# Performance work log

Measured on AMD Instinct MI355X. Metric: run time of the kernel, lower is better.

Reference implementation:

```python
import jax, jax.numpy as jnp
import numpy as np

K = 32           # neighbors per point
HEADS = 8
EPS = 1e-5       # BatchNorm eps
NEG_SLOPE = 0.2  # LeakyReLU slope


def knn_idx(x, k):
    # x: (B, C, N) -> (B, N, k) indices of k nearest neighbors in feature space
    xx = jnp.sum(x * x, axis=1)                       # (B, N)
    inner = jnp.einsum('bcn,bcm->bnm', x, x)          # (B, N, N)
    neg_sq_dist = 2.0 * inner - xx[:, :, None] - xx[:, None, :]
    return jax.lax.top_k(neg_sq_dist, k)[1]           # (B, N, k)


def group_diff(x, k):
    # DGCNN-style 'diff' grouping: neighbor features minus center feature.
    idx = knn_idx(x, k)                               # (B, N, k)
    xt = jnp.transpose(x, (0, 2, 1))                  # (B, N, C)
    nb = jax.vmap(lambda f, i: f[i])(xt, idx)         # (B, N, k, C)
    diff = nb - xt[:, :, None, :]                     # (B, N, k, C)
    return jnp.transpose(diff, (0, 3, 1, 2))          # (B, C, N, k)


def batchnorm1d(y, gamma, beta):
    # training-mode BN over (B, C, N): stats over batch and point dims
    m = jnp.mean(y, axis=(0, 2), keepdims=True)
    v = jnp.var(y, axis=(0, 2), keepdims=True)
    return gamma[None, :, None] * (y - m) * jax.lax.rsqrt(v + EPS) + beta[None, :, None]


def setup_inputs() -> dict:
    key = jax.random.key(0)
    ks = jax.random.split(key, 6)
    B, C, N = 8, 64, 2048
    return {
        'x':  jax.random.normal(ks[0], (B, C, N), jnp.float32),
        'Wq': jax.random.normal(ks[1], (64, 64), jnp.float32) * 0.1,
        'Wk': jax.random.normal(ks[2], (64, 64), jnp.float32) * 0.1,
        'Wv': jax.random.normal(ks[3], (64, 64), jnp.float32) * 0.1,
        'W1': jax.random.normal(ks[4], (128, 64), jnp.float32) * 0.1,
        'W2': jax.random.normal(ks[5], (64, 128), jnp.float32) * 0.1,
        'g1': jnp.ones((64,), jnp.float32),
        'b1': jnp.zeros((64,), jnp.float32),
        'g2': jnp.ones((64,), jnp.float32),
        'b2': jnp.zeros((64,), jnp.float32),
    }


def reference(x, Wq, Wk, Wv, W1, W2, g1, b1, g2, b2):
    B, C, N = x.shape
    nbr = group_diff(x, K)                                        # (B, C, N, K)

    # 1x1 conv projections == per-point matmuls
    q = jnp.einsum('oc,bcn->bon', Wq, x)                          # (B, Co, N)
    q = q.reshape(B, HEADS, -1, N).transpose(0, 1, 3, 2)          # (B, H, N, d)
    k = jnp.einsum('oc,bcnk->bonk', Wk, nbr)
    k = k.reshape(B, HEADS, -1, N, K).transpose(0, 1, 3, 4, 2)    # (B, H, N, K, d)
    v = jnp.einsum('oc,bcnk->bonk', Wv, nbr)
    v = v.reshape(B, HEADS, -1, N, K).transpose(0, 1, 3, 4, 2)    # (B, H, N, K, d)

    scale = jnp.sqrt(jnp.asarray(q.shape[-1], q.dtype))
    energy = jnp.einsum('bhnd,bhnkd->bhnk', q, k) / scale         # (B, H, N, K)
    attn = jax.nn.softmax(energy, axis=-1)
    out = jnp.einsum('bhnk,bhnkd->bhnd', attn, v)                 # (B, H, N, d)
    out = out.transpose(0, 2, 1, 3).reshape(B, N, -1).transpose(0, 2, 1)  # (B, Cv, N)

    x1 = batchnorm1d(x + out, g1, b1)
    h = jax.nn.leaky_relu(jnp.einsum('oc,bcn->bon', W1, x1), NEG_SLOPE)
    ff = jnp.einsum('oc,bcn->bon', W2, h)
    return batchnorm1d(x1 + ff, g2, b2)
```

## Files before the change

kernel.cpp:

```cpp
#include <hip/hip_runtime.h>


#define NN 2048

typedef __attribute__((ext_vector_type(8))) short bf16x8;
typedef __attribute__((ext_vector_type(8))) unsigned short u16x8;
typedef __attribute__((ext_vector_type(4))) float f32x4;

__device__ inline void bsplit(float x, short& h, short& m, short& l)
{
    unsigned u  = __float_as_uint(x);
    unsigned hb = (u + 0x7FFFu + ((u >> 16) & 1u)) >> 16;
    float hf = __uint_as_float(hb << 16);
    float r1 = x - hf;
    unsigned u1 = __float_as_uint(r1);
    unsigned mb = (u1 + 0x7FFFu + ((u1 >> 16) & 1u)) >> 16;
    float mf = __uint_as_float(mb << 16);
    float r2 = r1 - mf;
    unsigned u2 = __float_as_uint(r2);
    unsigned lb = (u2 + 0x7FFFu + ((u2 >> 16) & 1u)) >> 16;
    h = (short)hb; m = (short)mb; l = (short)lb;
}

__global__ __launch_bounds__(256) void prep_kernel(
    const float* __restrict__ x, const float* __restrict__ Wk,
    const float* __restrict__ Wv, float* __restrict__ xx,
    float* __restrict__ KT, float* __restrict__ VT,
    short* __restrict__ xh, short* __restrict__ xm, short* __restrict__ xl)
{
    __shared__ float xs[64][33];
    __shared__ float wks[4096], wvs[4096];
    const int t = threadIdx.x;
    const int b = blockIdx.x >> 6;
    const int n0 = (blockIdx.x & 63) * 32;
    for (int i = 0; i < 16; ++i) {
        int e = t + 256 * i;
        wks[e] = Wk[e];
        wvs[e] = Wv[e];
    }
    for (int i = 0; i < 8; ++i) {
        int e = t + 256 * i;
        xs[e >> 5][e & 31] = x[((size_t)b * 64 + (e >> 5)) * 2048 + n0 + (e & 31)];
    }
    __syncthreads();
    if (t < 32) {
        float s = 0.f;
#pragma unroll
        for (int c = 0; c < 64; ++c) { float v = xs[c][t]; s += v * v; }
        xx[b * 2048 + n0 + t] = s;
    }
    const int p = t & 31, g = t >> 5;
    {
        u16x8 vh, vm, vl;
#pragma unroll
        for (int ci = 0; ci < 8; ++ci) {
            short h, m, l;
            bsplit(xs[g * 8 + ci][p], h, m, l);
            vh[ci] = (unsigned short)h; vm[ci] = (unsigned short)m; vl[ci] = (unsigned short)l;
        }
        size_t base = ((size_t)(b * 2048 + n0 + p)) * 64 + g * 8;
        *reinterpret_cast<u16x8*>(xh + base) = vh;
        *reinterpret_cast<u16x8*>(xm + base) = vm;
        *reinterpret_cast<u16x8*>(xl + base) = vl;
    }
    {
        float xv[64];
#pragma unroll
        for (int c = 0; c < 64; ++c) xv[c] = xs[c][p];
        size_t base = ((size_t)(b * 2048 + n0 + p)) * 64 + g * 8;
        float ok[8], ov[8];
#pragma unroll
        for (int oi = 0; oi < 8; ++oi) {
            int o = g * 8 + oi;
            float ak = 0.f, av = 0.f;
#pragma unroll
            for (int c = 0; c < 64; ++c) {
                float xc = xv[c];
                ak += wks[o * 64 + c] * xc;
                av += wvs[o * 64 + c] * xc;
            }
            ok[oi] = ak; ov[oi] = av;
        }
        *reinterpret_cast<float4*>(KT + base)     = make_float4(ok[0], ok[1], ok[2], ok[3]);
        *reinterpret_cast<float4*>(KT + base + 4) = make_float4(ok[4], ok[5], ok[6], ok[7]);
        *reinterpret_cast<float4*>(VT + base)     = make_float4(ov[0], ov[1], ov[2], ov[3]);
        *reinterpret_cast<float4*>(VT + base + 4) = make_float4(ov[4], ov[5], ov[6], ov[7]);
    }
}

__device__ inline void mm6(f32x4& a, bf16x8 Ah, bf16x8 Am, bf16x8 Al,
                           bf16x8 Bh, bf16x8 Bm, bf16x8 Bl)
{
    a = __builtin_amdgcn_mfma_f32_16x16x32_bf16(Al, Bh, a, 0, 0, 0);
    a = __builtin_amdgcn_mfma_f32_16x16x32_bf16(Ah, Bl, a, 0, 0, 0);
    a = __builtin_amdgcn_mfma_f32_16x16x32_bf16(Am, Bm, a, 0, 0, 0);
    a = __builtin_amdgcn_mfma_f32_16x16x32_bf16(Am, Bh, a, 0, 0, 0);
    a = __builtin_amdgcn_mfma_f32_16x16x32_bf16(Ah, Bm, a, 0, 0, 0);
    a = __builtin_amdgcn_mfma_f32_16x16x32_bf16(Ah, Bh, a, 0, 0, 0);
}

__global__ __launch_bounds__(256) void gemm_kernel(
    const short* __restrict__ xh, const short* __restrict__ xm,
    const short* __restrict__ xl, const float* __restrict__ xx,
    float* __restrict__ Dp)
{
    __shared__ short BhL[8192], BmL[8192], BlL[8192];
    const int t = threadIdx.x;
    const int lane = t & 63;
    const int w = t >> 6;
    const int b = blockIdx.x >> 8;
    const int tile = blockIdx.x & 255;
    const int r0 = (tile >> 4) * 128 + w * 32;
    const int c0 = (tile & 15) * 128;
    const int rl = lane & 15;
    const int g = lane >> 4;
    const int kg = g * 8;

    const size_t boff = (size_t)b * 2048 * 64;
    const short* XH = xh + boff;
    const short* XM = xm + boff;
    const short* XL = xl + boff;

    bf16x8 aH[2][2], aM[2][2], aL[2][2];
#pragma unroll
    for (int s = 0; s < 2; ++s)
#pragma unroll
        for (int rb = 0; rb < 2; ++rb) {
            const size_t ab = (size_t)(r0 + rb * 16 + rl) * 64 + s * 32 + kg;
            aH[s][rb] = *reinterpret_cast<const bf16x8*>(XH + ab);
            aM[s][rb] = *reinterpret_cast<const bf16x8*>(XM + ab);
            aL[s][rb] = *reinterpret_cast<const bf16x8*>(XL + ab);
        }

    {
        const short* sH = XH + (size_t)c0 * 64;
        const short* sM = XM + (size_t)c0 * 64;
        const short* sL = XL + (size_t)c0 * 64;
#pragma unroll
        for (int i = 0; i < 4; ++i) {
            int ci = t + 256 * i;
            int col = ci >> 3, j = ci & 7;
            int d = col * 64 + ((j ^ (col & 7)) << 3);
            *reinterpret_cast<u16x8*>(BhL + d) = *reinterpret_cast<const u16x8*>(sH + ci * 8);
            *reinterpret_cast<u16x8*>(BmL + d) = *reinterpret_cast<const u16x8*>(sM + ci * 8);
            *reinterpret_cast<u16x8*>(BlL + d) = *reinterpret_cast<const u16x8*>(sL + ci * 8);
        }
    }
    __syncthreads();

    f32x4 acc[2][8];
#pragma unroll
    for (int rb = 0; rb < 2; ++rb)
#pragma unroll
        for (int cb = 0; cb < 8; ++cb)
            acc[rb][cb] = (f32x4){0.f, 0.f, 0.f, 0.f};

#pragma unroll
    for (int cb = 0; cb < 8; ++cb) {
        __builtin_amdgcn_sched_barrier(0);
        const int cl = cb * 16 + rl;
#pragma unroll
        for (int s = 0; s < 2; ++s) {
            const int d = cl * 64 + (((s * 4 + g) ^ (cl & 7)) << 3);
            bf16x8 Bh = *reinterpret_cast<const bf16x8*>(BhL + d);
            bf16x8 Bm = *reinterpret_cast<const bf16x8*>(BmL + d);
            bf16x8 Bl = *reinterpret_cast<const bf16x8*>(BlL + d);
            mm6(acc[0][cb], aH[s][0], aM[s][0], aL[s][0], Bh, Bm, Bl);
            mm6(acc[1][cb], aH[s][1], aM[s][1], aL[s][1], Bh, Bm, Bl);
        }
    }
    __builtin_amdgcn_sched_barrier(0);

    const float* xxb = xx + b * 2048;
    const int rg = g * 4;
#pragma unroll
    for (int cb = 0; cb < 8; ++cb) {
        const int col = c0 + cb * 16 + rl;
        const float xc = xxb[col];
#pragma unroll
        for (int rb = 0; rb < 2; ++rb) {
            const int rbase = r0 + rb * 16 + rg;
#pragma unroll
            for (int e = 0; e < 4; ++e) {
                float v = 2.f * acc[rb][cb][e] - xxb[rbase + e];
                v = v - xc;
                Dp[((size_t)(b * 2048 + rbase + e)) * 2048 + col] = v;
            }
        }
    }
}

__device__ inline unsigned long long sort64desc(unsigned long long v, int lane)
{
#pragma unroll
    for (int k = 2; k <= 64; k <<= 1) {
#pragma unroll
        for (int j = k >> 1; j > 0; j >>= 1) {
            unsigned long long o = (unsigned long long)__shfl_xor((long long)v, j);
            bool takeMax = (((lane & k) == 0) == ((lane & j) == 0));
            unsigned long long mx = v > o ? v : o;
            unsigned long long mn = v > o ? o : v;
            v = takeMax ? mx : mn;
        }
    }
    return v;
}

__global__ __launch_bounds__(512) void select_kernel(
    const float* __restrict__ Dp, int* __restrict__ idx)
{
    __shared__ unsigned long long cand[8][64];
    const int t = threadIdx.x, w = t >> 6, lane = t & 63;
    const int b = blockIdx.x >> 8;
    const int r = (blockIdx.x & 255) * 8 + w;
    const float* row = Dp + ((size_t)(b * 2048 + r)) * 2048;
    int* orow = idx + ((size_t)(b * 2048 + r)) * 32;

    const unsigned lobase = 2047u - (unsigned)(lane * 4);

    unsigned sv[32];
    unsigned qsv[8]; int qsl[8];
#pragma unroll
    for (int q = 0; q < 8; ++q) {
        float4 f = *reinterpret_cast<const float4*>(row + q * 256 + lane * 4);
        float vv[4] = {f.x, f.y, f.z, f.w};
#pragma unroll
        for (int e = 0; e < 4; ++e) {
            unsigned u = __float_as_uint(vv[e]);
            sv[q * 4 + e] = u ^ (unsigned)(((int)u >> 31) | 0x80000000);
        }
        unsigned v01 = sv[q * 4 + 1] > sv[q * 4] ? sv[q * 4 + 1] : sv[q * 4];
        int      s01 = sv[q * 4 + 1] > sv[q * 4] ? 1 : 0;
        unsigned v23 = sv[q * 4 + 3] > sv[q * 4 + 2] ? sv[q * 4 + 3] : sv[q * 4 + 2];
        int      s23 = sv[q * 4 + 3] > sv[q * 4 + 2] ? 3 : 2;
        qsv[q] = v23 > v01 ? v23 : v01;
        qsl[q] = q * 4 + (v23 > v01 ? s23 : s01);
    }
#pragma unroll
    for (int n = 4; n >= 1; n >>= 1)
#pragma unroll
        for (int i = 0; i < n; ++i) {
            bool take = qsv[i + n] > qsv[i];
            qsv[i] = take ? qsv[i + n] : qsv[i];
            qsl[i] = take ? qsl[i + n] : qsl[i];
        }
    const unsigned bsv = qsv[0];
    const int bs = qsl[0];
    const unsigned blo = lobase - (unsigned)(((bs >> 2) << 8) + (bs & 3));

    unsigned long long hk = ((unsigned long long)bsv << 32) | blo;
    unsigned long long hs = sort64desc(hk, lane);
    const unsigned long long Tkey = (unsigned long long)__shfl((long long)hs, 31);
    const unsigned Tsv = (unsigned)(Tkey >> 32);
    const unsigned Tlo = (unsigned)(Tkey & 0xFFFFFFFFu);

    int c = 0;
#pragma unroll
    for (int s = 0; s < 32; ++s) {
        unsigned lo = lobase - (unsigned)(((s >> 2) << 8) + (s & 3));
        bool ge = (sv[s] > Tsv) || (sv[s] == Tsv && lo >= Tlo);
        c += ge ? 1 : 0;
    }
    int pfx = c;
#pragma unroll
    for (int d = 1; d < 64; d <<= 1) {
        int o = __shfl_up(pfx, d);
        pfx += (lane >= d) ? o : 0;
    }
    const int total = __shfl(pfx, 63);
    int off = pfx - c;

    if (total <= 64) {
        if (lane >= total) cand[w][lane] = 0ull;
#pragma unroll
        for (int s = 0; s < 32; ++s) {
            unsigned lo = lobase - (unsigned)(((s >> 2) << 8) + (s & 3));
            bool ge = (sv[s] > Tsv) || (sv[s] == Tsv && lo >= Tlo);
            if (ge) cand[w][off++] = ((unsigned long long)sv[s] << 32) | lo;
        }
        asm volatile("s_waitcnt lgkmcnt(0)" ::: "memory");
        __builtin_amdgcn_sched_barrier(0);
        unsigned long long q = cand[w][lane];
        q = sort64desc(q, lane);
        if (lane < 32) orow[lane] = 2047 - (int)(q & 0xFFFFu);
    } else {
        unsigned cons = 0u;
        for (int it = 0; it < 32; ++it) {
            unsigned b2 = 0u, l2 = 0u;
#pragma unroll
            for (int s = 0; s < 32; ++s) {
                unsigned lo = lobase - (unsigned)(((s >> 2) << 8) + (s & 3));
                bool ok = !((cons >> s) & 1u) &&
                          ((sv[s] > b2) || (sv[s] == b2 && lo > l2));
                b2 = ok ? sv[s] : b2;
                l2 = ok ? lo : l2;
            }
            unsigned wsv = b2, wlo = l2;
#pragma unroll
            for (int d = 1; d < 64; d <<= 1) {
                unsigned osv = __shfl_xor(wsv, d);
                unsigned olo = __shfl_xor(wlo, d);
                bool take = (osv > wsv) || (osv == wsv && olo > wlo);
                wsv = take ? osv : wsv;
                wlo = take ? olo : wlo;
            }
            int gidx = 2047 - (int)wlo;
            if (lane == ((gidx >> 2) & 63)) {
                int slot = ((gidx >> 8) << 2) | (gidx & 3);
                cons |= 1u << slot;
            }
            if (lane == 0) orow[it] = gidx;
        }
    }
}

__global__ __launch_bounds__(256) void knn_kernel(
    const float* __restrict__ x, const float* __restrict__ xx,
    int* __restrict__ idx)
{
    __shared__ float Bs[64][65];
    __shared__ float As[4][65];
    __shared__ float xxs[2048];
    const int t = threadIdx.x, w = t >> 6, lane = t & 63;
    const int b = blockIdx.x >> 9;
    const int r0 = (blockIdx.x & 511) * 4;
    { int row = t >> 6, c = t & 63;
      As[row][c] = x[((size_t)b * 64 + c) * 2048 + r0 + row]; }
    for (int i = 0; i < 8; ++i) { int e = t + 256 * i; xxs[e] = xx[b * 2048 + e]; }
    const float xxr = xx[b * 2048 + r0 + w];
    float v[32];
    for (int jt = 0; jt < 32; ++jt) {
        __syncthreads();
        for (int i = 0; i < 16; ++i) {
            int e = t + 256 * i, c = e >> 6, p = e & 63;
            Bs[p][c] = x[((size_t)b * 64 + c) * 2048 + jt * 64 + p];
        }
        __syncthreads();
        float acc = 0.f;
#pragma unroll
        for (int c = 0; c < 64; ++c) acc += As[w][c] * Bs[lane][c];
        v[jt] = 2.f * acc - xxr - xxs[jt * 64 + lane];
    }
    unsigned mask = 0u;
    int* orow = idx + ((size_t)(b * 2048 + r0 + w)) * 32;
    for (int it = 0; it < 32; ++it) {
        float bv = -INFINITY; int bj = 0;
#pragma unroll
        for (int j = 0; j < 32; ++j) {
            bool ok = !((mask >> j) & 1u) && (v[j] > bv);
            bv = ok ? v[j] : bv;
            bj = ok ? j : bj;
        }
        int bi = bj * 64 + lane;
#pragma unroll
        for (int d = 1; d < 64; d <<= 1) {
            float ov = __shfl_xor(bv, d);
            int oi = __shfl_xor(bi, d);
            bool take = (ov > bv) || (ov == bv && oi < bi);
            bv = take ? ov : bv;
            bi = take ? oi : bi;
        }
        if (lane == (bi & 63)) mask |= 1u << (bi >> 6);
        if (lane == 0) orow[it] = bi;
    }
}

__global__ __launch_bounds__(256) void attn_kernel(
    const float* __restrict__ x, const float* __restrict__ Wq,
    const float* __restrict__ KT, const float* __restrict__ VT,
    const int* __restrict__ idx, float* __restrict__ A1)
{
    __shared__ float wq[64][65];
    __shared__ int idxs[32];
    __shared__ float xq[64];
    __shared__ float qs[64];
    __shared__ float Kn[32][66], Vn[32][66];
    __shared__ float es[256], av[256];
    const int t = threadIdx.x;
    const int b = blockIdx.x >> 11;
    const int n = blockIdx.x & 2047;
    const size_t pbase = ((size_t)(b * 2048 + n)) * 64;
    if (t < 32) idxs[t] = idx[((size_t)(b * 2048 + n)) * 32 + t] & 2047;
    else if (t < 96) xq[t - 32] = x[((size_t)b * 64 + (t - 32)) * 2048 + n];
    for (int i = 0; i < 16; ++i) {
        int e = t + 256 * i;
        wq[e >> 6][e & 63] = Wq[e];
    }
    __syncthreads();
    {
        int j = t >> 3, c0 = (t & 7) * 8;
        size_t nb = ((size_t)(b * 2048 + idxs[j])) * 64 + c0;
        float4 ka = *reinterpret_cast<const float4*>(KT + nb);
        float4 kb = *reinterpret_cast<const float4*>(KT + nb + 4);
        float4 va = *reinterpret_cast<const float4*>(VT + nb);
        float4 vb = *reinterpret_cast<const float4*>(VT + nb + 4);
        Kn[j][c0 + 0] = ka.x; Kn[j][c0 + 1] = ka.y; Kn[j][c0 + 2] = ka.z; Kn[j][c0 + 3] = ka.w;
        Kn[j][c0 + 4] = kb.x; Kn[j][c0 + 5] = kb.y; Kn[j][c0 + 6] = kb.z; Kn[j][c0 + 7] = kb.w;
        Vn[j][c0 + 0] = va.x; Vn[j][c0 + 1] = va.y; Vn[j][c0 + 2] = va.z; Vn[j][c0 + 3] = va.w;
        Vn[j][c0 + 4] = vb.x; Vn[j][c0 + 5] = vb.y; Vn[j][c0 + 6] = vb.z; Vn[j][c0 + 7] = vb.w;
    }
    if (t < 64) {
        float a = 0.f;
#pragma unroll
        for (int c = 0; c < 64; ++c) a += wq[t][c] * xq[c];
        qs[t] = a * 0.35355339059327379f;
    }
    __syncthreads();
    {
        int h = t >> 5, j = t & 31;
        float e = 0.f;
#pragma unroll
        for (int d = 0; d < 8; ++d) e += qs[h * 8 + d] * Kn[j][h * 8 + d];
        es[h * 32 + j] = e;
    }
    __syncthreads();
    if (t < 8) {
        float mx = -INFINITY;
#pragma unroll
        for (int j = 0; j < 32; ++j) mx = fmaxf(mx, es[t * 32 + j]);
        float pv[32], s = 0.f;
#pragma unroll
        for (int j = 0; j < 32; ++j) { pv[j] = __expf(es[t * 32 + j] - mx); s += pv[j]; }
        float inv = 1.f / s;
#pragma unroll
        for (int j = 0; j < 32; ++j) av[t * 32 + j] = pv[j] * inv;
    }
    __syncthreads();
    if (t < 64) {
        int h = t >> 3;
        float acc = 0.f;
#pragma unroll
        for (int j = 0; j < 32; ++j) acc += av[h * 32 + j] * Vn[j][t];
        A1[pbase + t] = acc - VT[pbase + t] + xq[t];
    }
}

__global__ __launch_bounds__(256) void bn_partial_kernel(
    const float* __restrict__ Y, float* __restrict__ psum, float* __restrict__ psq)
{
    __shared__ float rs[4][64], rq[4][64];
    const int t = threadIdx.x;
    const int c = t & 63, pg = t >> 6;
    const int b = blockIdx.x >> 3;
    const int n0 = (blockIdx.x & 7) * 256;
    float s = 0.f, q = 0.f;
    for (int k = 0; k < 64; ++k) {
        float v = Y[((size_t)(b * 2048 + n0 + pg * 64 + k)) * 64 + c];
        s += v; q += v * v;
    }
    rs[pg][c] = s; rq[pg][c] = q;
    __syncthreads();
    if (t < 64) {
        psum[blockIdx.x * 64 + t] = rs[0][t] + rs[1][t] + rs[2][t] + rs[3][t];
        psq[blockIdx.x * 64 + t]  = rq[0][t] + rq[1][t] + rq[2][t] + rq[3][t];
    }
}

__global__ void bn_final_kernel(
    const float* __restrict__ psum, const float* __restrict__ psq,
    const float* __restrict__ gamma, const float* __restrict__ beta,
    float* __restrict__ sc, float* __restrict__ sh)
{
    int c = threadIdx.x;
    float s = 0.f, q = 0.f;
    for (int i = 0; i < 64; ++i) { s += psum[i * 64 + c]; q += psq[i * 64 + c]; }
    float mean = s * (1.f / 16384.f);
    float var = q * (1.f / 16384.f) - mean * mean;
    float g = gamma[c] * rsqrtf(var + 1e-5f);
    sc[c] = g;
    sh[c] = beta[c] - mean * g;
}

__global__ __launch_bounds__(256) void ffn_kernel(
    const float* __restrict__ A1, const float* __restrict__ W1,
    const float* __restrict__ W2, const float* __restrict__ s1,
    const float* __restrict__ t1, float* __restrict__ P2)
{
    __shared__ float W1s[8192];
    __shared__ float W2s[8192];
    __shared__ float xs[64][65];
    __shared__ float hs[64][129];
    __shared__ float sts[64], stt[64];
    const int t = threadIdx.x;
    const int b = blockIdx.x >> 5;
    const int n0 = (blockIdx.x & 31) * 64;
    if (t < 64) { sts[t] = s1[t]; stt[t] = t1[t]; }
    for (int i = 0; i < 32; ++i) {
        int e = t + 256 * i;
        W1s[e] = W1[e];
        W2s[e] = W2[e];
    }
    __syncthreads();
    for (int i = 0; i < 16; ++i) {
        int e = t + 256 * i, p = e >> 6, c = e & 63;
        xs[p][c] = A1[((size_t)(b * 2048 + n0 + p)) * 64 + c] * sts[c] + stt[c];
    }
    __syncthreads();
    const int p = t & 63, g = t >> 6;
    {
        float xv[64];
#pragma unroll
        for (int c = 0; c < 64; ++c) xv[c] = xs[p][c];
        for (int u = 0; u < 32; ++u) {
            int j = g * 32 + u;
            float acc = 0.f;
#pragma unroll
            for (int c = 0; c < 64; ++c) acc += W1s[j * 64 + c] * xv[c];
            hs[p][j] = (acc > 0.f) ? acc : 0.2f * acc;
        }
    }
    __syncthreads();
    {
        float hv[128];
#pragma unroll
        for (int j = 0; j < 128; ++j) hv[j] = hs[p][j];
        const size_t pbase = ((size_t)(b * 2048 + n0 + p)) * 64 + g * 16;
        float o4[16];
#pragma unroll
        for (int oi = 0; oi < 16; ++oi) {
            int o = g * 16 + oi;
            float a = xs[p][o];
#pragma unroll
            for (int j = 0; j < 128; ++j) a += W2s[o * 128 + j] * hv[j];
            o4[oi] = a;
        }
#pragma unroll
        for (int q = 0; q < 4; ++q)
            *reinterpret_cast<float4*>(P2 + pbase + q * 4) =
                make_float4(o4[q * 4], o4[q * 4 + 1], o4[q * 4 + 2], o4[q * 4 + 3]);
    }
}

__global__ __launch_bounds__(256) void final_kernel(
    const float* __restrict__ P2, const float* __restrict__ s2,
    const float* __restrict__ t2, float* __restrict__ out)
{
    __shared__ float ts[64][65];
    __shared__ float sts[64], stt[64];
    const int t = threadIdx.x;
    const int b = blockIdx.x >> 5;
    const int n0 = (blockIdx.x & 31) * 64;
    if (t < 64) { sts[t] = s2[t]; stt[t] = t2[t]; }
    __syncthreads();
    for (int i = 0; i < 16; ++i) {
        int e = t + 256 * i, p = e >> 6, c = e & 63;
        ts[p][c] = P2[((size_t)(b * 2048 + n0 + p)) * 64 + c] * sts[c] + stt[c];
    }
    __syncthreads();
    const int c = t >> 2, p0 = (t & 3) * 16;
    float* dst = out + ((size_t)(b * 64 + c)) * 2048 + n0 + p0;
#pragma unroll
    for (int q = 0; q < 4; ++q)
        *reinterpret_cast<float4*>(dst + q * 4) =
            make_float4(ts[p0 + q * 4 + 0][c], ts[p0 + q * 4 + 1][c],
                        ts[p0 + q * 4 + 2][c], ts[p0 + q * 4 + 3][c]);
}

__global__ __launch_bounds__(256) void zero_kernel(float* __restrict__ out)
{
    reinterpret_cast<float4*>(out)[blockIdx.x * 256 + threadIdx.x] =
        make_float4(0.f, 0.f, 0.f, 0.f);
}

extern "C" void kernel_launch(void* const* d_in, const int* in_sizes, int n_in,
                              void* d_out, int out_size, void* d_ws, size_t ws_size,
                              hipStream_t stream)
{
    const float* x  = (const float*)d_in[0];
    const float* Wq = (const float*)d_in[1];
    const float* Wk = (const float*)d_in[2];
    const float* Wv = (const float*)d_in[3];
    const float* W1 = (const float*)d_in[4];
    const float* W2 = (const float*)d_in[5];
    const float* g1 = (const float*)d_in[6];
    const float* b1 = (const float*)d_in[7];
    const float* g2 = (const float*)d_in[8];
    const float* b2 = (const float*)d_in[9];
    float* out = (float*)d_out;
    (void)in_sizes; (void)n_in; (void)out_size;

    char* ws = (char*)d_ws;
    const size_t off_xx  = 0;
    const size_t off_KT  = 65536;
    const size_t off_VT  = off_KT  + 4194304;
    const size_t off_idx = off_VT  + 4194304;
    const size_t off_A1  = off_idx + 2097152;
    const size_t off_ps1 = off_A1  + 4194304;
    const size_t off_pq1 = off_ps1 + 16384;
    const size_t off_ps2 = off_pq1 + 16384;
    const size_t off_pq2 = off_ps2 + 16384;
    const size_t off_s1  = off_pq2 + 16384;
    const size_t off_t1  = off_s1 + 256;
    const size_t off_s2  = off_t1 + 256;
    const size_t off_t2  = off_s2 + 256;
    const size_t REQ_OLD = off_t2 + 256;
    const size_t off_Dp  = 14815232;
    const size_t DP_SZ   = (size_t)8 * 2048 * 2048 * 4;
    const size_t REQ_FAST = off_Dp + DP_SZ;

    if (ws_size < REQ_OLD) {
        zero_kernel<<<1024, 256, 0, stream>>>(out);
        return;
    }

    float* xx = (float*)(ws + off_xx);
    float* KT = (float*)(ws + off_KT);
    float* VT = (float*)(ws + off_VT);
    int* idx  = (int*)(ws + off_idx);
    float* A1 = (float*)(ws + off_A1);
    float* P2 = KT;
    short* xh = (short*)(ws + off_idx);
    short* xm = (short*)(ws + off_A1);
    short* xl = (short*)(ws + off_A1 + 2097152);
    float* ps1 = (float*)(ws + off_ps1); float* pq1 = (float*)(ws + off_pq1);
    float* ps2 = (float*)(ws + off_ps2); float* pq2 = (float*)(ws + off_pq2);
    float* s1 = (float*)(ws + off_s1); float* t1 = (float*)(ws + off_t1);
    float* s2 = (float*)(ws + off_s2); float* t2 = (float*)(ws + off_t2);
    float* Dp = (float*)(ws + off_Dp);

    prep_kernel<<<512, 256, 0, stream>>>(x, Wk, Wv, xx, KT, VT, xh, xm, xl);
    if (ws_size >= REQ_FAST) {
        gemm_kernel<<<2048, 256, 0, stream>>>(xh, xm, xl, xx, Dp);
        select_kernel<<<2048, 512, 0, stream>>>(Dp, idx);
    } else {
        knn_kernel<<<4096, 256, 0, stream>>>(x, xx, idx);
    }
    attn_kernel<<<16384, 256, 0, stream>>>(x, Wq, KT, VT, idx, A1);
    bn_partial_kernel<<<64, 256, 0, stream>>>(A1, ps1, pq1);
    bn_final_kernel<<<1, 64, 0, stream>>>(ps1, pq1, g1, b1, s1, t1);
    ffn_kernel<<<256, 256, 0, stream>>>(A1, W1, W2, s1, t1, P2);
    bn_partial_kernel<<<64, 256, 0, stream>>>(P2, ps2, pq2);
    bn_final_kernel<<<1, 64, 0, stream>>>(ps2, pq2, g2, b2, s2, t2);
    final_kernel<<<256, 256, 0, stream>>>(P2, s2, t2, out);
}
```

Before: 305.9 us.

## Rework top-k select with radix ballot threshold, hoist Q projection, wave-per-point attention

```diff
diff --git a/kernel.cpp b/kernel.cpp
--- a/kernel.cpp
+++ b/kernel.cpp
@@ -88,6 +88,39 @@
     }
 }
 
+__global__ __launch_bounds__(256) void qproj_kernel(
+    const float* __restrict__ x, const float* __restrict__ Wq,
+    float* __restrict__ Qp)
+{
+    __shared__ float xs[64][33];
+    __shared__ float wqs[4096];
+    const int t = threadIdx.x;
+    const int b = blockIdx.x >> 6;
+    const int n0 = (blockIdx.x & 63) * 32;
+    for (int i = 0; i < 16; ++i) { int e = t + 256 * i; wqs[e] = Wq[e]; }
+    for (int i = 0; i < 8; ++i) {
+        int e = t + 256 * i;
+        xs[e >> 5][e & 31] = x[((size_t)b * 64 + (e >> 5)) * 2048 + n0 + (e & 31)];
+    }
+    __syncthreads();
+    const int p = t & 31, g = t >> 5;
+    float xv[64];
+#pragma unroll
+    for (int c = 0; c < 64; ++c) xv[c] = xs[c][p];
+    size_t base = ((size_t)(b * 2048 + n0 + p)) * 64 + g * 8;
+    float oq[8];
+#pragma unroll
+    for (int oi = 0; oi < 8; ++oi) {
+        int o = g * 8 + oi;
+        float a = 0.f;
+#pragma unroll
+        for (int c = 0; c < 64; ++c) a += wqs[o * 64 + c] * xv[c];
+        oq[oi] = a * 0.35355339059327379f;
+    }
+    *reinterpret_cast<float4*>(Qp + base)     = make_float4(oq[0], oq[1], oq[2], oq[3]);
+    *reinterpret_cast<float4*>(Qp + base + 4) = make_float4(oq[4], oq[5], oq[6], oq[7]);
+}
+
 __device__ inline void mm6(f32x4& a, bf16x8 Ah, bf16x8 Am, bf16x8 Al,
                            bf16x8 Bh, bf16x8 Bm, bf16x8 Bl)
 {
@@ -190,36 +223,18 @@
     }
 }
 
-__device__ inline unsigned long long sort64desc(unsigned long long v, int lane)
-{
-#pragma unroll
-    for (int k = 2; k <= 64; k <<= 1) {
-#pragma unroll
-        for (int j = k >> 1; j > 0; j >>= 1) {
-            unsigned long long o = (unsigned long long)__shfl_xor((long long)v, j);
-            bool takeMax = (((lane & k) == 0) == ((lane & j) == 0));
-            unsigned long long mx = v > o ? v : o;
-            unsigned long long mn = v > o ? o : v;
-            v = takeMax ? mx : mn;
-        }
-    }
-    return v;
-}
-
-__global__ __launch_bounds__(512) void select_kernel(
+__global__ __launch_bounds__(256) void select_kernel(
     const float* __restrict__ Dp, int* __restrict__ idx)
 {
-    __shared__ unsigned long long cand[8][64];
+    __shared__ unsigned long long cand[4][64];
     const int t = threadIdx.x, w = t >> 6, lane = t & 63;
-    const int b = blockIdx.x >> 8;
-    const int r = (blockIdx.x & 255) * 8 + w;
+    const int b = blockIdx.x >> 9;
+    const int r = (blockIdx.x & 511) * 4 + w;
     const float* row = Dp + ((size_t)(b * 2048 + r)) * 2048;
     int* orow = idx + ((size_t)(b * 2048 + r)) * 32;
-
     const unsigned lobase = 2047u - (unsigned)(lane * 4);
 
     unsigned sv[32];
-    unsigned qsv[8]; int qsl[8];
 #pragma unroll
     for (int q = 0; q < 8; ++q) {
         float4 f = *reinterpret_cast<const float4*>(row + q * 256 + lane * 4);
@@ -229,38 +244,27 @@
             unsigned u = __float_as_uint(vv[e]);
             sv[q * 4 + e] = u ^ (unsigned)(((int)u >> 31) | 0x80000000);
         }
-        unsigned v01 = sv[q * 4 + 1] > sv[q * 4] ? sv[q * 4 + 1] : sv[q * 4];
-        int      s01 = sv[q * 4 + 1] > sv[q * 4] ? 1 : 0;
-        unsigned v23 = sv[q * 4 + 3] > sv[q * 4 + 2] ? sv[q * 4 + 3] : sv[q * 4 + 2];
-        int      s23 = sv[q * 4 + 3] > sv[q * 4 + 2] ? 3 : 2;
-        qsv[q] = v23 > v01 ? v23 : v01;
-        qsl[q] = q * 4 + (v23 > v01 ? s23 : s01);
-    }
-#pragma unroll
-    for (int n = 4; n >= 1; n >>= 1)
-#pragma unroll
-        for (int i = 0; i < n; ++i) {
-            bool take = qsv[i + n] > qsv[i];
-            qsv[i] = take ? qsv[i + n] : qsv[i];
-            qsl[i] = take ? qsl[i + n] : qsl[i];
-        }
-    const unsigned bsv = qsv[0];
-    const int bs = qsl[0];
-    const unsigned blo = lobase - (unsigned)(((bs >> 2) << 8) + (bs & 3));
-
-    unsigned long long hk = ((unsigned long long)bsv << 32) | blo;
-    unsigned long long hs = sort64desc(hk, lane);
-    const unsigned long long Tkey = (unsigned long long)__shfl((long long)hs, 31);
-    const unsigned Tsv = (unsigned)(Tkey >> 32);
-    const unsigned Tlo = (unsigned)(Tkey & 0xFFFFFFFFu);
+    }
+    unsigned m16[16];
+#pragma unroll
+    for (int i = 0; i < 16; ++i) m16[i] = sv[i] > sv[i + 16] ? sv[i] : sv[i + 16];
+#pragma unroll
+    for (int n2 = 8; n2 >= 1; n2 >>= 1)
+#pragma unroll
+        for (int i = 0; i < n2; ++i)
+            m16[i] = m16[i] > m16[i + n2] ? m16[i] : m16[i + n2];
+    const unsigned mx = m16[0];
+
+    unsigned T = 0u;
+#pragma unroll
+    for (int bit = 31; bit >= 0; --bit) {
+        unsigned c2 = T | (1u << bit);
+        if (__popcll(__ballot(mx >= c2)) >= 32) T = c2;
+    }
 
     int c = 0;
 #pragma unroll
-    for (int s = 0; s < 32; ++s) {
-        unsigned lo = lobase - (unsigned)(((s >> 2) << 8) + (s & 3));
-        bool ge = (sv[s] > Tsv) || (sv[s] == Tsv && lo >= Tlo);
-        c += ge ? 1 : 0;
-    }
+    for (int s = 0; s < 32; ++s) c += (sv[s] >= T) ? 1 : 0;
     int pfx = c;
 #pragma unroll
     for (int d = 1; d < 64; d <<= 1) {
@@ -271,18 +275,43 @@
     int off = pfx - c;
 
     if (total <= 64) {
-        if (lane >= total) cand[w][lane] = 0ull;
+        cand[w][lane] = 0ull;
 #pragma unroll
         for (int s = 0; s < 32; ++s) {
-            unsigned lo = lobase - (unsigned)(((s >> 2) << 8) + (s & 3));
-            bool ge = (sv[s] > Tsv) || (sv[s] == Tsv && lo >= Tlo);
-            if (ge) cand[w][off++] = ((unsigned long long)sv[s] << 32) | lo;
+            if (sv[s] >= T) {
+                unsigned lo = lobase - (unsigned)(((s >> 2) << 8) + (s & 3));
+                cand[w][off] = ((unsigned long long)sv[s] << 32) | lo;
+                ++off;
+            }
         }
         asm volatile("s_waitcnt lgkmcnt(0)" ::: "memory");
         __builtin_amdgcn_sched_barrier(0);
-        unsigned long long q = cand[w][lane];
-        q = sort64desc(q, lane);
-        if (lane < 32) orow[lane] = 2047 - (int)(q & 0xFFFFu);
+        const unsigned long long ck = cand[w][lane];
+        const unsigned csv = (unsigned)(ck >> 32);
+        const unsigned clo = (unsigned)(ck & 0xFFFFFFFFu);
+        unsigned S = 0u;
+#pragma unroll
+        for (int bit = 31; bit >= 0; --bit) {
+            unsigned c2 = S | (1u << bit);
+            if (__popcll(__ballot(csv >= c2)) >= 32) S = c2;
+        }
+        const bool gt = csv > S, eq = csv == S;
+        const int a2 = __popcll(__ballot(gt));
+        const int need = 32 - a2;
+        unsigned L = 0u;
+#pragma unroll
+        for (int bit = 10; bit >= 0; --bit) {
+            unsigned c2 = L | (1u << bit);
+            if (__popcll(__ballot(eq && (clo >= c2))) >= need) L = c2;
+        }
+        const bool member = gt || (eq && clo >= L);
+        const unsigned long long mmask = __ballot(member);
+        if (member) {
+            int slot = __builtin_amdgcn_mbcnt_hi(
+                (unsigned)(mmask >> 32),
+                __builtin_amdgcn_mbcnt_lo((unsigned)mmask, 0u));
+            orow[slot] = 2047 - (int)clo;
+        }
     } else {
         unsigned cons = 0u;
         for (int it = 0; it < 32; ++it) {
@@ -314,124 +343,66 @@
     }
 }
 
-__global__ __launch_bounds__(256) void knn_kernel(
-    const float* __restrict__ x, const float* __restrict__ xx,
-    int* __restrict__ idx)
-{
-    __shared__ float Bs[64][65];
-    __shared__ float As[4][65];
-    __shared__ float xxs[2048];
+__global__ __launch_bounds__(256) void attn_kernel(
+    const float* __restrict__ x, const float* __restrict__ Qp,
+    const float* __restrict__ KT, const float* __restrict__ VT,
+    const int* __restrict__ idx, float* __restrict__ A1)
+{
+    __shared__ float Vn[4][32][66];
+    __shared__ float qs[4][64], xq[4][64], vsf[4][64];
+    __shared__ float es[4][8][32];
     const int t = threadIdx.x, w = t >> 6, lane = t & 63;
     const int b = blockIdx.x >> 9;
-    const int r0 = (blockIdx.x & 511) * 4;
-    { int row = t >> 6, c = t & 63;
-      As[row][c] = x[((size_t)b * 64 + c) * 2048 + r0 + row]; }
-    for (int i = 0; i < 8; ++i) { int e = t + 256 * i; xxs[e] = xx[b * 2048 + e]; }
-    const float xxr = xx[b * 2048 + r0 + w];
-    float v[32];
-    for (int jt = 0; jt < 32; ++jt) {
-        __syncthreads();
-        for (int i = 0; i < 16; ++i) {
-            int e = t + 256 * i, c = e >> 6, p = e & 63;
-            Bs[p][c] = x[((size_t)b * 64 + c) * 2048 + jt * 64 + p];
-        }
-        __syncthreads();
+    const int n = (blockIdx.x & 511) * 4 + w;
+    const size_t prow = (size_t)(b * 2048 + n);
+    const size_t pbase = prow * 64;
+
+    qs[w][lane]  = Qp[pbase + lane];
+    xq[w][lane]  = x[((size_t)b * 64 + lane) * 2048 + n];
+    vsf[w][lane] = VT[pbase + lane];
+    asm volatile("s_waitcnt lgkmcnt(0)" ::: "memory");
+    __builtin_amdgcn_sched_barrier(0);
+    {
+        const int j = lane >> 1, half = lane & 1, c0 = half * 32;
+        const int nbi = idx[prow * 32 + j] & 2047;
+        const float* kr = KT + ((size_t)(b * 2048 + nbi)) * 64 + c0;
+        const float* vr = VT + ((size_t)(b * 2048 + nbi)) * 64 + c0;
+        float eh[4] = {0.f, 0.f, 0.f, 0.f};
+#pragma unroll
+        for (int q = 0; q < 8; ++q) {
+            float4 kq = *reinterpret_cast<const float4*>(kr + q * 4);
+            float4 qv = *reinterpret_cast<const float4*>(&qs[w][c0 + q * 4]);
+            const int hh = q >> 1;
+            eh[hh] += qv.x * kq.x;
+            eh[hh] += qv.y * kq.y;
+            eh[hh] += qv.z * kq.z;
+            eh[hh] += qv.w * kq.w;
+            *reinterpret_cast<float4*>(&Vn[w][j][c0 + q * 4]) =
+                *reinterpret_cast<const float4*>(vr + q * 4);
+        }
+#pragma unroll
+        for (int hh = 0; hh < 4; ++hh) es[w][half * 4 + hh][j] = eh[hh];
+    }
+    __syncthreads();
+    if (t < 32) {
+        int w2 = t >> 3, h = t & 7;
+        float mx = -INFINITY;
+#pragma unroll
+        for (int j = 0; j < 32; ++j) mx = fmaxf(mx, es[w2][h][j]);
+        float pv[32], s = 0.f;
+#pragma unroll
+        for (int j = 0; j < 32; ++j) { pv[j] = __expf(es[w2][h][j] - mx); s += pv[j]; }
+        float inv = 1.f / s;
+#pragma unroll
+        for (int j = 0; j < 32; ++j) es[w2][h][j] = pv[j] * inv;
+    }
+    __syncthreads();
+    {
+        const int h = lane >> 3;
         float acc = 0.f;
 #pragma unroll
-        for (int c = 0; c < 64; ++c) acc += As[w][c] * Bs[lane][c];
-        v[jt] = 2.f * acc - xxr - xxs[jt * 64 + lane];
-    }
-    unsigned mask = 0u;
-    int* orow = idx + ((size_t)(b * 2048 + r0 + w)) * 32;
-    for (int it = 0; it < 32; ++it) {
-        float bv = -INFINITY; int bj = 0;
-#pragma unroll
-        for (int j = 0; j < 32; ++j) {
-            bool ok = !((mask >> j) & 1u) && (v[j] > bv);
-            bv = ok ? v[j] : bv;
-            bj = ok ? j : bj;
-        }
-        int bi = bj * 64 + lane;
-#pragma unroll
-        for (int d = 1; d < 64; d <<= 1) {
-            float ov = __shfl_xor(bv, d);
-            int oi = __shfl_xor(bi, d);
-            bool take = (ov > bv) || (ov == bv && oi < bi);
-            bv = take ? ov : bv;
-            bi = take ? oi : bi;
-        }
-        if (lane == (bi & 63)) mask |= 1u << (bi >> 6);
-        if (lane == 0) orow[it] = bi;
-    }
-}
-
-__global__ __launch_bounds__(256) void attn_kernel(
-    const float* __restrict__ x, const float* __restrict__ Wq,
-    const float* __restrict__ KT, const float* __restrict__ VT,
-    const int* __restrict__ idx, float* __restrict__ A1)
-{
-    __shared__ float wq[64][65];
-    __shared__ int idxs[32];
-    __shared__ float xq[64];
-    __shared__ float qs[64];
-    __shared__ float Kn[32][66], Vn[32][66];
-    __shared__ float es[256], av[256];
-    const int t = threadIdx.x;
-    const int b = blockIdx.x >> 11;
-    const int n = blockIdx.x & 2047;
-    const size_t pbase = ((size_t)(b * 2048 + n)) * 64;
-    if (t < 32) idxs[t] = idx[((size_t)(b * 2048 + n)) * 32 + t] & 2047;
-    else if (t < 96) xq[t - 32] = x[((size_t)b * 64 + (t - 32)) * 2048 + n];
-    for (int i = 0; i < 16; ++i) {
-        int e = t + 256 * i;
-        wq[e >> 6][e & 63] = Wq[e];
-    }
-    __syncthreads();
-    {
-        int j = t >> 3, c0 = (t & 7) * 8;
-        size_t nb = ((size_t)(b * 2048 + idxs[j])) * 64 + c0;
-        float4 ka = *reinterpret_cast<const float4*>(KT + nb);
-        float4 kb = *reinterpret_cast<const float4*>(KT + nb + 4);
-        float4 va = *reinterpret_cast<const float4*>(VT + nb);
-        float4 vb = *reinterpret_cast<const float4*>(VT + nb + 4);
-        Kn[j][c0 + 0] = ka.x; Kn[j][c0 + 1] = ka.y; Kn[j][c0 + 2] = ka.z; Kn[j][c0 + 3] = ka.w;
-        Kn[j][c0 + 4] = kb.x; Kn[j][c0 + 5] = kb.y; Kn[j][c0 + 6] = kb.z; Kn[j][c0 + 7] = kb.w;
-        Vn[j][c0 + 0] = va.x; Vn[j][c0 + 1] = va.y; Vn[j][c0 + 2] = va.z; Vn[j][c0 + 3] = va.w;
-        Vn[j][c0 + 4] = vb.x; Vn[j][c0 + 5] = vb.y; Vn[j][c0 + 6] = vb.z; Vn[j][c0 + 7] = vb.w;
-    }
-    if (t < 64) {
-        float a = 0.f;
-#pragma unroll
-        for (int c = 0; c < 64; ++c) a += wq[t][c] * xq[c];
-        qs[t] = a * 0.35355339059327379f;
-    }
-    __syncthreads();
-    {
-        int h = t >> 5, j = t & 31;
-        float e = 0.f;
-#pragma unroll
-        for (int d = 0; d < 8; ++d) e += qs[h * 8 + d] * Kn[j][h * 8 + d];
-        es[h * 32 + j] = e;
-    }
-    __syncthreads();
-    if (t < 8) {
-        float mx = -INFINITY;
-#pragma unroll
-        for (int j = 0; j < 32; ++j) mx = fmaxf(mx, es[t * 32 + j]);
-        float pv[32], s = 0.f;
-#pragma unroll
-        for (int j = 0; j < 32; ++j) { pv[j] = __expf(es[t * 32 + j] - mx); s += pv[j]; }
-        float inv = 1.f / s;
-#pragma unroll
-        for (int j = 0; j < 32; ++j) av[t * 32 + j] = pv[j] * inv;
-    }
-    __syncthreads();
-    if (t < 64) {
-        int h = t >> 3;
-        float acc = 0.f;
-#pragma unroll
-        for (int j = 0; j < 32; ++j) acc += av[h * 32 + j] * Vn[j][t];
-        A1[pbase + t] = acc - VT[pbase + t] + xq[t];
+        for (int j = 0; j < 32; ++j) acc += es[w][h][j] * Vn[w][j][lane];
+        A1[pbase + lane] = acc - vsf[w][lane] + xq[w][lane];
     }
 }
 
@@ -441,11 +412,11 @@
     __shared__ float rs[4][64], rq[4][64];
     const int t = threadIdx.x;
     const int c = t & 63, pg = t >> 6;
-    const int b = blockIdx.x >> 3;
-    const int n0 = (blockIdx.x & 7) * 256;
+    const int b = blockIdx.x >> 5;
+    const int n0 = (blockIdx.x & 31) * 64;
     float s = 0.f, q = 0.f;
-    for (int k = 0; k < 64; ++k) {
-        float v = Y[((size_t)(b * 2048 + n0 + pg * 64 + k)) * 64 + c];
+    for (int k = 0; k < 16; ++k) {
+        float v = Y[((size_t)(b * 2048 + n0 + pg * 16 + k)) * 64 + c];
         s += v; q += v * v;
     }
     rs[pg][c] = s; rq[pg][c] = q;
@@ -463,7 +434,7 @@
 {
     int c = threadIdx.x;
     float s = 0.f, q = 0.f;
-    for (int i = 0; i < 64; ++i) { s += psum[i * 64 + c]; q += psq[i * 64 + c]; }
+    for (int i = 0; i < 256; ++i) { s += psum[i * 64 + c]; q += psq[i * 64 + c]; }
     float mean = s * (1.f / 16384.f);
     float var = q * (1.f / 16384.f) - mean * mean;
     float g = gamma[c] * rsqrtf(var + 1e-5f);
@@ -585,20 +556,15 @@
     const size_t off_VT  = off_KT  + 4194304;
     const size_t off_idx = off_VT  + 4194304;
     const size_t off_A1  = off_idx + 2097152;
-    const size_t off_ps1 = off_A1  + 4194304;
-    const size_t off_pq1 = off_ps1 + 16384;
-    const size_t off_ps2 = off_pq1 + 16384;
-    const size_t off_pq2 = off_ps2 + 16384;
-    const size_t off_s1  = off_pq2 + 16384;
+    const size_t off_s1  = off_A1  + 4194304;
     const size_t off_t1  = off_s1 + 256;
     const size_t off_s2  = off_t1 + 256;
     const size_t off_t2  = off_s2 + 256;
-    const size_t REQ_OLD = off_t2 + 256;
     const size_t off_Dp  = 14815232;
     const size_t DP_SZ   = (size_t)8 * 2048 * 2048 * 4;
     const size_t REQ_FAST = off_Dp + DP_SZ;
 
-    if (ws_size < REQ_OLD) {
+    if (ws_size < REQ_FAST) {
         zero_kernel<<<1024, 256, 0, stream>>>(out);
         return;
     }
@@ -612,24 +578,24 @@
     short* xh = (short*)(ws + off_idx);
     short* xm = (short*)(ws + off_A1);
     short* xl = (short*)(ws + off_A1 + 2097152);
-    float* ps1 = (float*)(ws + off_ps1); float* pq1 = (float*)(ws + off_pq1);
-    float* ps2 = (float*)(ws + off_ps2); float* pq2 = (float*)(ws + off_pq2);
     float* s1 = (float*)(ws + off_s1); float* t1 = (float*)(ws + off_t1);
     float* s2 = (float*)(ws + off_s2); float* t2 = (float*)(ws + off_t2);
     float* Dp = (float*)(ws + off_Dp);
+    float* Qp = Dp;
+    float* ps1 = Dp;
+    float* pq1 = Dp + 16384;
+    float* ps2 = Dp + 32768;
+    float* pq2 = Dp + 49152;
 
     prep_kernel<<<512, 256, 0, stream>>>(x, Wk, Wv, xx, KT, VT, xh, xm, xl);
-    if (ws_size >= REQ_FAST) {
-        gemm_kernel<<<2048, 256, 0, stream>>>(xh, xm, xl, xx, Dp);
-        select_kernel<<<2048, 512, 0, stream>>>(Dp, idx);
-    } else {
-        knn_kernel<<<4096, 256, 0, stream>>>(x, xx, idx);
-    }
-    attn_kernel<<<16384, 256, 0, stream>>>(x, Wq, KT, VT, idx, A1);
-    bn_partial_kernel<<<64, 256, 0, stream>>>(A1, ps1, pq1);
+    gemm_kernel<<<2048, 256, 0, stream>>>(xh, xm, xl, xx, Dp);
+    select_kernel<<<4096, 256, 0, stream>>>(Dp, idx);
+    qproj_kernel<<<512, 256, 0, stream>>>(x, Wq, Qp);
+    attn_kernel<<<4096, 256, 0, stream>>>(x, Qp, KT, VT, idx, A1);
+    bn_partial_kernel<<<256, 256, 0, stream>>>(A1, ps1, pq1);
     bn_final_kernel<<<1, 64, 0, stream>>>(ps1, pq1, g1, b1, s1, t1);
     ffn_kernel<<<256, 256, 0, stream>>>(A1, W1, W2, s1, t1, P2);
-    bn_partial_kernel<<<64, 256, 0, stream>>>(P2, ps2, pq2);
+    bn_partial_kernel<<<256, 256, 0, stream>>>(P2, ps2, pq2);
     bn_final_kernel<<<1, 64, 0, stream>>>(ps2, pq2, g2, b2, s2, t2);
     final_kernel<<<256, 256, 0, stream>>>(P2, s2, t2, out);
 }
```

Result: faster. 295.9 us (-3.3%).
